# Optimization experiments

Hardware: AMD Instinct MI355X
Metric: run time of the kernel (lower is better)

## Reference

```python
import jax, jax.numpy as jnp
import numpy as np

B, T, D, H = 4, 1024, 1024, 16
DH = D // H
BETA = 0.9


def setup_inputs() -> dict:
    key = jax.random.key(0)
    ks = jax.random.split(key, 9)
    s = 1.0 / np.sqrt(D)
    return {
        "x": jax.random.normal(ks[0], (B, T, D), jnp.float32),
        "l3_memory": jax.random.normal(ks[1], (B, 1, D), jnp.float32),
        "wq": jax.random.normal(ks[2], (D, D), jnp.float32) * s,
        "wk": jax.random.normal(ks[3], (D, D), jnp.float32) * s,
        "wv": jax.random.normal(ks[4], (D, D), jnp.float32) * s,
        "wo": jax.random.normal(ks[5], (D, D), jnp.float32) * s,
        "rw1": jax.random.normal(ks[6], (D, D // 2), jnp.float32) * s,
        "rb1": jnp.zeros((D // 2,), jnp.float32),
        "rw2": jax.random.normal(ks[7], (D // 2, 3), jnp.float32) * (1.0 / np.sqrt(D // 2)),
        "rb2": jnp.zeros((3,), jnp.float32),
    }


def reference(x, l3_memory, wq, wk, wv, wo, rw1, rb1, rw2, rb2):
    b, t, d = x.shape
    dh = d // H

    def heads(y):  # [b,t,d] -> [b,h,t,dh]
        return y.reshape(b, t, H, dh).transpose(0, 2, 1, 3)

    q = x @ wq
    qh = heads(q)

    # L2: causal prefix EMA along time: y_t = beta*y_{t-1} + (1-beta)*x_t, y_{-1}=0
    def ema_step(c, xt):
        y = BETA * c + (1.0 - BETA) * xt
        return y, y
    _, l2 = jax.lax.scan(ema_step, jnp.zeros((b, d), x.dtype), jnp.swapaxes(x, 0, 1))
    l2 = jnp.swapaxes(l2, 0, 1)

    # L3: retrieval memory repeated to sequence length
    l3 = jnp.broadcast_to(l3_memory, (b, t, d))

    mask = jnp.tril(jnp.ones((t, t), bool))
    neg = jnp.finfo(x.dtype).min
    scale = 1.0 / np.sqrt(dh)

    def attend(mem):
        kh = heads(mem @ wk)
        vh = heads(mem @ wv)
        s = jnp.einsum('bhqd,bhkd->bhqk', qh, kh) * scale
        s = jnp.where(mask[None, None], s, neg)
        p = jax.nn.softmax(s, axis=-1)
        return jnp.einsum('bhqk,bhkd->bhqd', p, vh)

    # router over q tokens -> softmax mixture weights [b,t,3]
    hdn = jax.nn.gelu(q @ rw1 + rb1, approximate=False)
    lam = jax.nn.softmax(hdn @ rw2 + rb2, axis=-1)

    mixed = jnp.zeros((b, H, t, dh), x.dtype)
    for i, mem in enumerate((x, l2, l3)):
        mixed = mixed + lam[:, None, :, i:i + 1] * attend(mem)

    out = mixed.transpose(0, 2, 1, 3).reshape(b, t, d) @ wo
    return out, lam
```

## Files before the change

### kernel.cpp

```cpp
#include <hip/hip_runtime.h>
#include <hip/hip_bf16.h>
#include <math.h>


#define B_ 4
#define T_ 1024
#define D_ 1024
#define H_ 16
#define DH_ 64
#define M_ 4096

#define ECH 16
#define NCH 64

typedef __attribute__((ext_vector_type(8))) short bf16x8;
typedef __attribute__((ext_vector_type(4))) short s16x4;
typedef __attribute__((ext_vector_type(4))) float f32x4;

__device__ inline short f2b(float f) {
  __hip_bfloat16 h = __float2bfloat16(f);
  return *reinterpret_cast<short*>(&h);
}

__device__ inline void gload_lds16(const short* g, short* l) {
  __builtin_amdgcn_global_load_lds(
      (const __attribute__((address_space(1))) unsigned int*)g,
      (__attribute__((address_space(3))) unsigned int*)l, 16, 0, 0);
}

__global__ __launch_bounds__(256) void ema_chunk_kernel(const float* __restrict__ x,
                                                        float* __restrict__ l2,
                                                        short* __restrict__ xb) {
  int idx = blockIdx.x * 256 + threadIdx.x;
  int d = idx & (D_ - 1);
  int ch = (idx >> 10) & (NCH - 1);
  int b = idx >> 16;
  const float* xp = x + (size_t)(b * T_ + ch * ECH) * D_ + d;
  float* yp = l2 + (size_t)(b * T_ + ch * ECH) * D_ + d;
  short* xbp = xb + (size_t)(b * T_ + ch * ECH) * D_ + d;
  float y = 0.f;
#pragma unroll 4
  for (int t = 0; t < ECH; ++t) {
    float xv = xp[t * D_];
    y = 0.9f * y + 0.1f * xv;
    yp[t * D_] = y;
    xbp[t * D_] = f2b(xv);
  }
}

__global__ __launch_bounds__(256) void ema_carry_kernel(const float* __restrict__ l2,
                                                        float* __restrict__ g) {
  int idx = blockIdx.x * 256 + threadIdx.x;
  int d = idx & (D_ - 1);
  int b = idx >> 10;
  const float bE = 0.1853020188851841f;
  float G = 0.f;
  for (int ch = 0; ch < NCH; ++ch) {
    g[(size_t)(b * NCH + ch) * D_ + d] = G;
    float lf = l2[(size_t)(b * T_ + ch * ECH + ECH - 1) * D_ + d];
    G = lf + bE * G;
  }
}

__global__ __launch_bounds__(256) void ema_fix_kernel(const float* __restrict__ l2,
                                                      const float* __restrict__ g,
                                                      short* __restrict__ l2b) {
  int idx = blockIdx.x * 256 + threadIdx.x;
  int d = idx & (D_ - 1);
  int t = (idx >> 10) & (T_ - 1);
  int b = idx >> 20;
  int ch = t / ECH;
  int off = t & (ECH - 1);
  float G = g[(size_t)(b * NCH + ch) * D_ + d];
  float p9 = exp2f((float)(off + 1) * -0.15200309344504997f);
  l2b[idx] = f2b(l2[idx] + p9 * G);
}

__global__ __launch_bounds__(256) void transpose_w_kernel(
    const float* __restrict__ w0, const float* __restrict__ w1,
    const float* __restrict__ w2, const float* __restrict__ w3,
    const float* __restrict__ w4,
    short* __restrict__ t0, short* __restrict__ t1, short* __restrict__ t2,
    short* __restrict__ t3, short* __restrict__ t4) {
  int z = blockIdx.z;
  const float* W = (z == 0) ? w0 : (z == 1) ? w1 : (z == 2) ? w2 : (z == 3) ? w3 : w4;
  short* Wt = (z == 0) ? t0 : (z == 1) ? t1 : (z == 2) ? t2 : (z == 3) ? t3 : t4;
  int cols = (z == 4) ? 512 : 1024;
  int c0 = blockIdx.x * 32, r0 = blockIdx.y * 32;
  if (c0 >= cols) return;
  __shared__ float tile[32][33];
  int tc = threadIdx.x & 31, tr8 = threadIdx.x >> 5;
#pragma unroll
  for (int i = 0; i < 4; ++i)
    tile[tr8 + i * 8][tc] = W[(size_t)(r0 + tr8 + i * 8) * cols + c0 + tc];
  __syncthreads();
#pragma unroll
  for (int i = 0; i < 4; ++i) {
    int rr = tr8 + i * 8;
    Wt[(size_t)(c0 + rr) * 1024 + r0 + tc] = f2b(tile[tc][rr]);
  }
}

template <int NB>
__global__ __launch_bounds__(256) void gemm_bt(const short* __restrict__ A, int lda,
                                               const short* __restrict__ Bt,
                                               float* __restrict__ Cf,
                                               short* __restrict__ Cb,
                                               int Ndim, int Kdim) {
  __shared__ short As[128 * 64];
  __shared__ short Bs[NB * 64];
  constexpr int NW = NB / 64;
  constexpr int NF = 4;
  constexpr int MF = (NW == 2) ? 4 : 2;
  int tid = threadIdx.x;
  int w = tid >> 6, l = tid & 63;
  int lg = l >> 4, ll = l & 15;
  int wr = (NW == 2) ? (w >> 1) : w;
  int wc = (NW == 2) ? (w & 1) : 0;
  int row0 = blockIdx.y * 128, col0 = blockIdx.x * NB;

  f32x4 acc[MF][NF];
#pragma unroll
  for (int m = 0; m < MF; ++m)
#pragma unroll
    for (int n = 0; n < NF; ++n) acc[m][n] = (f32x4){0.f, 0.f, 0.f, 0.f};

  for (int k0 = 0; k0 < Kdim; k0 += 64) {
    __syncthreads();
#pragma unroll
    for (int it = 0; it < 4; ++it) {
      int s = it * 256 + w * 64 + l;
      int r = s >> 3;
      int c = (s & 7) ^ (r & 7);
      gload_lds16(A + (size_t)(row0 + r) * lda + k0 + c * 8, &As[(it * 256 + w * 64) * 8]);
    }
#pragma unroll
    for (int it = 0; it < NB / 32; ++it) {
      int s = it * 256 + w * 64 + l;
      int r = s >> 3;
      int c = (s & 7) ^ (r & 7);
      gload_lds16(Bt + (size_t)(col0 + r) * Kdim + k0 + c * 8, &Bs[(it * 256 + w * 64) * 8]);
    }
    __syncthreads();
#pragma unroll
    for (int ks = 0; ks < 2; ++ks) {
      bf16x8 af[MF], bfr[NF];
#pragma unroll
      for (int m = 0; m < MF; ++m) {
        int r = wr * (MF * 16) + m * 16 + ll;
        af[m] = *(const bf16x8*)&As[r * 64 + (((ks * 4 + lg) ^ (r & 7)) << 3)];
      }
#pragma unroll
      for (int n = 0; n < NF; ++n) {
        int r = wc * 64 + n * 16 + ll;
        bfr[n] = *(const bf16x8*)&Bs[r * 64 + (((ks * 4 + lg) ^ (r & 7)) << 3)];
      }
#pragma unroll
      for (int m = 0; m < MF; ++m)
#pragma unroll
        for (int n = 0; n < NF; ++n)
          acc[m][n] = __builtin_amdgcn_mfma_f32_16x16x32_bf16(af[m], bfr[n], acc[m][n], 0, 0, 0);
    }
  }
#pragma unroll
  for (int m = 0; m < MF; ++m) {
    int gr = row0 + wr * (MF * 16) + m * 16 + lg * 4;
#pragma unroll
    for (int n = 0; n < NF; ++n) {
      int gc = col0 + wc * 64 + n * 16 + ll;
#pragma unroll
      for (int r = 0; r < 4; ++r) {
        float vv = acc[m][n][r];
        if (Cf) Cf[(size_t)(gr + r) * Ndim + gc] = vv;
        if (Cb) Cb[(size_t)(gr + r) * Ndim + gc] = f2b(vv);
      }
    }
  }
}

__global__ __launch_bounds__(256) void gemm_dual(const short* __restrict__ xb,
                                                 const short* __restrict__ l2b,
                                                 const short* __restrict__ wqkvT,
                                                 short* __restrict__ QKV,
                                                 short* __restrict__ KV2) {
  int lin = blockIdx.y * 40 + blockIdx.x;
  int lin2 = (lin & 7) * 160 + (lin >> 3);
  int bx = lin2 % 40;
  int by = lin2 / 40;

  const short* A;
  const short* Bt;
  short* Cb;
  int Ndim, col0;
  if (bx < 24) {
    A = xb; Bt = wqkvT; Cb = QKV; Ndim = 3072; col0 = bx * 128;
  } else {
    A = l2b; Bt = wqkvT + 1024 * 1024; Cb = KV2; Ndim = 2048; col0 = (bx - 24) * 128;
  }
  __shared__ short As[128 * 64];
  __shared__ short Bs[128 * 64];
  int tid = threadIdx.x;
  int w = tid >> 6, l = tid & 63;
  int lg = l >> 4, ll = l & 15;
  int wr = w >> 1, wc = w & 1;
  int row0 = by * 128;

  f32x4 acc[4][4];
#pragma unroll
  for (int m = 0; m < 4; ++m)
#pragma unroll
    for (int n = 0; n < 4; ++n) acc[m][n] = (f32x4){0.f, 0.f, 0.f, 0.f};

  for (int k0 = 0; k0 < 1024; k0 += 64) {
    __syncthreads();
#pragma unroll
    for (int it = 0; it < 4; ++it) {
      int s = it * 256 + w * 64 + l;
      int r = s >> 3;
      int c = (s & 7) ^ (r & 7);
      gload_lds16(A + (size_t)(row0 + r) * 1024 + k0 + c * 8, &As[(it * 256 + w * 64) * 8]);
      gload_lds16(Bt + (size_t)(col0 + r) * 1024 + k0 + c * 8, &Bs[(it * 256 + w * 64) * 8]);
    }
    __syncthreads();
#pragma unroll
    for (int ks = 0; ks < 2; ++ks) {
      bf16x8 af[4], bfr[4];
#pragma unroll
      for (int m = 0; m < 4; ++m) {
        int r = wr * 64 + m * 16 + ll;
        af[m] = *(const bf16x8*)&As[r * 64 + (((ks * 4 + lg) ^ (r & 7)) << 3)];
      }
#pragma unroll
      for (int n = 0; n < 4; ++n) {
        int r = wc * 64 + n * 16 + ll;
        bfr[n] = *(const bf16x8*)&Bs[r * 64 + (((ks * 4 + lg) ^ (r & 7)) << 3)];
      }
#pragma unroll
      for (int m = 0; m < 4; ++m)
#pragma unroll
        for (int n = 0; n < 4; ++n)
          acc[m][n] = __builtin_amdgcn_mfma_f32_16x16x32_bf16(af[m], bfr[n], acc[m][n], 0, 0, 0);
    }
  }
#pragma unroll
  for (int m = 0; m < 4; ++m) {
    int gr = row0 + wr * 64 + m * 16 + lg * 4;
#pragma unroll
    for (int n = 0; n < 4; ++n) {
      int gc = col0 + wc * 64 + n * 16 + ll;
#pragma unroll
      for (int r = 0; r < 4; ++r)
        Cb[(size_t)(gr + r) * Ndim + gc] = f2b(acc[m][n][r]);
    }
  }
}

__global__ __launch_bounds__(256) void v3_kernel(const float* __restrict__ l3,
                                                 const float* __restrict__ wv,
                                                 float* __restrict__ v3) {
  int idx = blockIdx.x * 256 + threadIdx.x;
  int b = idx >> 10;
  int col = idx & 1023;
  const float* xr = l3 + (size_t)b * D_;
  float acc = 0.f;
#pragma unroll 8
  for (int k = 0; k < D_; ++k) acc += xr[k] * wv[(size_t)k * D_ + col];
  v3[idx] = acc;
}

__global__ __launch_bounds__(256) void router_kernel(const float* __restrict__ hdnp,
                                                     const float* __restrict__ rb1,
                                                     const float* __restrict__ rw2,
                                                     const float* __restrict__ rb2,
                                                     float* __restrict__ lam) {
  int wave = (blockIdx.x * 256 + threadIdx.x) >> 6;
  int lane = threadIdx.x & 63;
  const float* hr = hdnp + (size_t)wave * 512;
  float s0 = 0.f, s1 = 0.f, s2 = 0.f;
#pragma unroll
  for (int u = 0; u < 8; ++u) {
    int hcol = u * 64 + lane;
    float vv = hr[hcol] + rb1[hcol];
    float gl = 0.5f * vv * (1.0f + erff(vv * 0.70710678118654752f));
    s0 += gl * rw2[hcol * 3 + 0];
    s1 += gl * rw2[hcol * 3 + 1];
    s2 += gl * rw2[hcol * 3 + 2];
  }
#pragma unroll
  for (int off = 32; off; off >>= 1) {
    s0 += __shfl_xor(s0, off);
    s1 += __shfl_xor(s1, off);
    s2 += __shfl_xor(s2, off);
  }
  if (lane == 0) {
    float a = s0 + rb2[0], bb = s1 + rb2[1], c = s2 + rb2[2];
    float m = fmaxf(fmaxf(a, bb), c);
    float e0 = expf(a - m), e1 = expf(bb - m), e2 = expf(c - m);
    float inv = 1.0f / (e0 + e1 + e2);
    lam[(size_t)wave * 3 + 0] = e0 * inv;
    lam[(size_t)wave * 3 + 1] = e1 * inv;
    lam[(size_t)wave * 3 + 2] = e2 * inv;
  }
}

__global__ __launch_bounds__(256) void attn_fused_kernel(
    const short* __restrict__ q, int ldq,
    const short* __restrict__ k1, const short* __restrict__ v1, int ld1,
    const short* __restrict__ k2, const short* __restrict__ v2, int ld2,
    const float* __restrict__ lam, const float* __restrict__ v3,
    short* __restrict__ mixedb) {
  __shared__ short Ks[2][64][64];
  __shared__ short Vt[2][64][64];
  __shared__ short Ps[4][16][64];

  int bid = blockIdx.x;
  int half = bid >> 9, p = bid & 511;
  int bh = p & 63;
  int j = p >> 6;
  int qb = half ? (15 - j) : j;
  int b = bh >> 4, h = bh & 15;
  int q0 = qb * 64;
  int tid = threadIdx.x;
  int w = tid >> 6, l = tid & 63;
  int lg = l >> 4, ll = l & 15;

  int qw0 = q0 + w * 16;
  bf16x8 qf[2];
  {
    const short* qr = q + (size_t)(b * T_ + qw0 + ll) * ldq + h * DH_;
    qf[0] = *(const bf16x8*)&qr[lg * 8];
    qf[1] = *(const bf16x8*)&qr[32 + lg * 8];
  }

  float m_[2][4];
  f32x4 o[2][4];
  f32x4 ol[2];
#pragma unroll
  for (int s = 0; s < 2; ++s) {
#pragma unroll
    for (int r = 0; r < 4; ++r) m_[s][r] = -1e30f;
#pragma unroll
    for (int db = 0; db < 4; ++db) o[s][db] = (f32x4){0.f, 0.f, 0.f, 0.f};
    ol[s] = (f32x4){0.f, 0.f, 0.f, 0.f};
  }

  bf16x8 ones;
#pragma unroll
  for (int jj = 0; jj < 8; ++jj) ones[jj] = (short)0x3F80;

  const float SC = 0.125f * 1.44269504f;
  int nt = qb + 1;
  for (int t64 = 0; t64 < nt; ++t64) {
    int key0 = t64 * 64;
    __syncthreads();
#pragma unroll
    for (int s = 0; s < 2; ++s) {
      const short* kp = s ? k2 : k1;
      const short* vp = s ? v2 : v1;
      int ld = s ? ld2 : ld1;
#pragma unroll
      for (int it = 0; it < 2; ++it) {
        int e = it * 256 + w * 64 + l;
        int r = e >> 3;
        int cs = (e & 7) ^ (r & 7);
        gload_lds16(kp + (size_t)(b * T_ + key0 + r) * ld + h * DH_ + cs * 8,
                    (short*)Ks[s] + (it * 256 + w * 64) * 8);
      }
      {
        int kp2 = tid >> 3, c8 = tid & 7;
        size_t gi = (size_t)(b * T_ + key0 + kp2 * 2) * ld + h * DH_ + c8 * 8;
        bf16x8 va = *(const bf16x8*)&vp[gi];
        bf16x8 vb = *(const bf16x8*)&vp[gi + ld];
        unsigned int* Vtd = (unsigned int*)Vt[s];
#pragma unroll
        for (int jj = 0; jj < 8; ++jj) {
          int dh = c8 * 8 + jj;
          int X = ((dh ^ (dh >> 3)) & 7) << 2;
          Vtd[dh * 32 + (kp2 ^ X)] =
              ((unsigned int)(unsigned short)va[jj]) |
              (((unsigned int)(unsigned short)vb[jj]) << 16);
        }
      }
    }
    __syncthreads();
    if (key0 > qw0 + 15) continue;

#pragma unroll
    for (int s = 0; s < 2; ++s) {
      f32x4 c[4];
#pragma unroll
      for (int kt = 0; kt < 4; ++kt) c[kt] = (f32x4){0.f, 0.f, 0.f, 0.f};
      __builtin_amdgcn_s_setprio(1);
#pragma unroll
      for (int kt = 0; kt < 4; ++kt) {
        int kr = kt * 16 + ll;
        bf16x8 kfa = *(const bf16x8*)&Ks[s][kr][((lg ^ (kr & 7)) << 3)];
        bf16x8 kfb = *(const bf16x8*)&Ks[s][kr][(((4 + lg) ^ (kr & 7)) << 3)];
        c[kt] = __builtin_amdgcn_mfma_f32_16x16x32_bf16(qf[0], kfa, c[kt], 0, 0, 0);
        c[kt] = __builtin_amdgcn_mfma_f32_16x16x32_bf16(qf[1], kfb, c[kt], 0, 0, 0);
      }
      __builtin_amdgcn_s_setprio(0);

      float sv[4][4];
      if (key0 + 63 <= qw0) {
#pragma unroll
        for (int r = 0; r < 4; ++r)
#pragma unroll
          for (int kt = 0; kt < 4; ++kt) sv[r][kt] = c[kt][r] * SC;
      } else {
#pragma unroll
        for (int r = 0; r < 4; ++r) {
          int grow = qw0 + lg * 4 + r;
#pragma unroll
          for (int kt = 0; kt < 4; ++kt) {
            float t = c[kt][r] * SC;
            sv[r][kt] = (key0 + kt * 16 + ll > grow) ? -1e30f : t;
          }
        }
      }

      float mx[4];
#pragma unroll
      for (int r = 0; r < 4; ++r) {
        float m0 = fmaxf(fmaxf(sv[r][0], sv[r][1]), fmaxf(sv[r][2], sv[r][3]));
        m0 = fmaxf(m0, __shfl_xor(m0, 1));
        m0 = fmaxf(m0, __shfl_xor(m0, 2));
        m0 = fmaxf(m0, __shfl_xor(m0, 4));
        m0 = fmaxf(m0, __shfl_xor(m0, 8));
        mx[r] = m0;
      }
      int grew = 0;
#pragma unroll
      for (int r = 0; r < 4; ++r) grew |= (mx[r] > m_[s][r] + 8.f) ? 1 : 0;
      if (__any(grew)) {
#pragma unroll
        for (int r = 0; r < 4; ++r) {
          float nm = fmaxf(m_[s][r], mx[r]);
          float al = exp2f(m_[s][r] - nm);
          m_[s][r] = nm;
          ol[s][r] *= al;
#pragma unroll
          for (int db = 0; db < 4; ++db) o[s][db][r] *= al;
        }
      }

#pragma unroll
      for (int r = 0; r < 4; ++r) {
        float mr = m_[s][r];
        int prow = lg * 4 + r;
#pragma unroll
        for (int kt = 0; kt < 4; ++kt) {
          float pv = exp2f(sv[r][kt] - mr);
          Ps[w][prow][((kt ^ lg) << 4) + ll] = f2b(pv);
        }
      }
      asm volatile("s_waitcnt lgkmcnt(0)" ::: "memory");
      __builtin_amdgcn_sched_barrier(0);

      __builtin_amdgcn_s_setprio(1);
#pragma unroll
      for (int ks = 0; ks < 2; ++ks) {
        int pswz = (ks * 32 + lg * 8) ^ ((ll >> 2) << 4);
        bf16x8 pf = *(const bf16x8*)&Ps[w][ll][pswz];
        const unsigned int* Vtd = (const unsigned int*)Vt[s];
        ol[s] = __builtin_amdgcn_mfma_f32_16x16x32_bf16(pf, ones, ol[s], 0, 0, 0);
#pragma unroll
        for (int db = 0; db < 4; ++db) {
          int dh = db * 16 + ll;
          int X = ((dh ^ (dh >> 3)) & 7) << 2;
          bf16x8 vf = *(const bf16x8*)&Vtd[dh * 32 + ((ks * 16 + lg * 4) ^ X)];
          o[s][db] = __builtin_amdgcn_mfma_f32_16x16x32_bf16(pf, vf, o[s][db], 0, 0, 0);
        }
      }
      __builtin_amdgcn_s_setprio(0);
      __builtin_amdgcn_sched_barrier(0);
    }
  }

#pragma unroll
  for (int r = 0; r < 4; ++r) {
    int grow = qw0 + lg * 4 + r;
    const float* lr = lam + (size_t)(b * T_ + grow) * 3;
    float w0 = lr[0] / ol[0][r];
    float w1 = lr[1] / ol[1][r];
    float w2 = lr[2];
#pragma unroll
    for (int db = 0; db < 4; ++db) {
      int dcol = h * DH_ + db * 16 + ll;
      float val = w0 * o[0][db][r] + w1 * o[1][db][r] + w2 * v3[(b << 10) + dcol];
      mixedb[(size_t)(b * T_ + grow) * D_ + dcol] = f2b(val);
    }
  }
}

extern "C" void kernel_launch(void* const* d_in, const int* in_sizes, int n_in,
                              void* d_out, int out_size, void* d_ws, size_t ws_size,
                              hipStream_t stream) {
  const float* x = (const float*)d_in[0];
  const float* l3m = (const float*)d_in[1];
  const float* wq = (const float*)d_in[2];
  const float* wk = (const float*)d_in[3];
  const float* wv = (const float*)d_in[4];
  const float* wo = (const float*)d_in[5];
  const float* rw1 = (const float*)d_in[6];
  const float* rb1 = (const float*)d_in[7];
  const float* rw2 = (const float*)d_in[8];
  const float* rb2 = (const float*)d_in[9];

  float* out = (float*)d_out;
  float* lam = out + (size_t)M_ * D_;

  float* ws = (float*)d_ws;
  float* l2 = ws;
  short* QKV = (short*)ws;
  float* hdnp = ws + 6291456;
  float* v3 = ws + 8388608;
  float* gbuf = ws + 8392704;
  short* sb = (short*)(ws + 8654848);
  short* xb = sb;
  short* l2b = sb + 4194304;
  short* KV2 = sb + 8388608;
  short* mixedb = sb + 16777216;
  short* wqkvT = sb + 20971520;
  short* woT = sb + 24117248;
  short* rw1T = sb + 25165824;

  dim3 blk(256);

  transpose_w_kernel<<<dim3(32, 32, 5), blk, 0, stream>>>(
      wq, wk, wv, wo, rw1,
      wqkvT, wqkvT + 1024 * 1024, wqkvT + 2048 * 1024, woT, rw1T);

  ema_chunk_kernel<<<1024, blk, 0, stream>>>(x, l2, xb);
  ema_carry_kernel<<<16, blk, 0, stream>>>(l2, gbuf);
  ema_fix_kernel<<<16384, blk, 0, stream>>>(l2, gbuf, l2b);

  gemm_dual<<<dim3(40, 32), blk, 0, stream>>>(xb, l2b, wqkvT, QKV, KV2);

  gemm_bt<64><<<dim3(8, 32), blk, 0, stream>>>(QKV, 3072, rw1T, hdnp, (short*)nullptr, 512, 1024);
  router_kernel<<<1024, blk, 0, stream>>>(hdnp, rb1, rw2, rb2, lam);

  v3_kernel<<<16, blk, 0, stream>>>(l3m, wv, v3);

  attn_fused_kernel<<<1024, blk, 0, stream>>>(QKV, 3072,
                                              QKV + 1024, QKV + 2048, 3072,
                                              KV2, KV2 + 1024, 2048,
                                              lam, v3, mixedb);

  gemm_bt<64><<<dim3(16, 32), blk, 0, stream>>>(mixedb, 1024, woT, out, (short*)nullptr, 1024, 1024);
}
```

Before: 251.2 us.

## Split two-memory attention across separate blocks and sum partial outputs

The fused attention kernel now handles a single memory source (x or EMA) per block, doubling the grid to 2048 blocks. Each block keeps half the LDS and accumulator registers, which should raise occupancy and parallelism. The cost is that the two partial mixtures are written to separate bf16 buffers and combined by an extra elementwise add kernel before the output GEMM, adding memory traffic and one more bf16 rounding.

```diff
diff --git a/kernel.cpp b/kernel.cpp
--- a/kernel.cpp
+++ b/kernel.cpp
@@ -20,6 +20,11 @@
 __device__ inline short f2b(float f) {
   __hip_bfloat16 h = __float2bfloat16(f);
   return *reinterpret_cast<short*>(&h);
+}
+
+__device__ inline float b2f(unsigned short u) {
+  unsigned int x = ((unsigned int)u) << 16;
+  return *reinterpret_cast<float*>(&x);
 }
 
 __device__ inline void gload_lds16(const short* g, short* l) {
@@ -308,13 +313,15 @@
     const short* __restrict__ k1, const short* __restrict__ v1, int ld1,
     const short* __restrict__ k2, const short* __restrict__ v2, int ld2,
     const float* __restrict__ lam, const float* __restrict__ v3,
-    short* __restrict__ mixedb) {
-  __shared__ short Ks[2][64][64];
-  __shared__ short Vt[2][64][64];
+    short* __restrict__ mix0, short* __restrict__ mix1) {
+  __shared__ short Ks[64][64];
+  __shared__ short Vt[64][64];
   __shared__ short Ps[4][16][64];
 
   int bid = blockIdx.x;
-  int half = bid >> 9, p = bid & 511;
+  int s = bid >> 10;
+  int bid2 = bid & 1023;
+  int half = bid2 >> 9, p = bid2 & 511;
   int bh = p & 63;
   int j = p >> 6;
   int qb = half ? (15 - j) : j;
@@ -324,6 +331,10 @@
   int w = tid >> 6, l = tid & 63;
   int lg = l >> 4, ll = l & 15;
 
+  const short* kp = s ? k2 : k1;
+  const short* vp = s ? v2 : v1;
+  int ld = s ? ld2 : ld1;
+
   int qw0 = q0 + w * 16;
   bf16x8 qf[2];
   {
@@ -332,17 +343,14 @@
     qf[1] = *(const bf16x8*)&qr[32 + lg * 8];
   }
 
-  float m_[2][4];
-  f32x4 o[2][4];
-  f32x4 ol[2];
-#pragma unroll
-  for (int s = 0; s < 2; ++s) {
-#pragma unroll
-    for (int r = 0; r < 4; ++r) m_[s][r] = -1e30f;
-#pragma unroll
-    for (int db = 0; db < 4; ++db) o[s][db] = (f32x4){0.f, 0.f, 0.f, 0.f};
-    ol[s] = (f32x4){0.f, 0.f, 0.f, 0.f};
-  }
+  float m_[4];
+  f32x4 o[4];
+  f32x4 ol;
+#pragma unroll
+  for (int r = 0; r < 4; ++r) m_[r] = -1e30f;
+#pragma unroll
+  for (int db = 0; db < 4; ++db) o[db] = (f32x4){0.f, 0.f, 0.f, 0.f};
+  ol = (f32x4){0.f, 0.f, 0.f, 0.f};
 
   bf16x8 ones;
 #pragma unroll
@@ -354,143 +362,149 @@
     int key0 = t64 * 64;
     __syncthreads();
 #pragma unroll
-    for (int s = 0; s < 2; ++s) {
-      const short* kp = s ? k2 : k1;
-      const short* vp = s ? v2 : v1;
-      int ld = s ? ld2 : ld1;
-#pragma unroll
-      for (int it = 0; it < 2; ++it) {
-        int e = it * 256 + w * 64 + l;
-        int r = e >> 3;
-        int cs = (e & 7) ^ (r & 7);
-        gload_lds16(kp + (size_t)(b * T_ + key0 + r) * ld + h * DH_ + cs * 8,
-                    (short*)Ks[s] + (it * 256 + w * 64) * 8);
-      }
-      {
-        int kp2 = tid >> 3, c8 = tid & 7;
-        size_t gi = (size_t)(b * T_ + key0 + kp2 * 2) * ld + h * DH_ + c8 * 8;
-        bf16x8 va = *(const bf16x8*)&vp[gi];
-        bf16x8 vb = *(const bf16x8*)&vp[gi + ld];
-        unsigned int* Vtd = (unsigned int*)Vt[s];
-#pragma unroll
-        for (int jj = 0; jj < 8; ++jj) {
-          int dh = c8 * 8 + jj;
-          int X = ((dh ^ (dh >> 3)) & 7) << 2;
-          Vtd[dh * 32 + (kp2 ^ X)] =
-              ((unsigned int)(unsigned short)va[jj]) |
-              (((unsigned int)(unsigned short)vb[jj]) << 16);
-        }
+    for (int it = 0; it < 2; ++it) {
+      int e = it * 256 + w * 64 + l;
+      int r = e >> 3;
+      int cs = (e & 7) ^ (r & 7);
+      gload_lds16(kp + (size_t)(b * T_ + key0 + r) * ld + h * DH_ + cs * 8,
+                  (short*)Ks + (it * 256 + w * 64) * 8);
+    }
+    {
+      int kp2 = tid >> 3, c8 = tid & 7;
+      size_t gi = (size_t)(b * T_ + key0 + kp2 * 2) * ld + h * DH_ + c8 * 8;
+      bf16x8 va = *(const bf16x8*)&vp[gi];
+      bf16x8 vb = *(const bf16x8*)&vp[gi + ld];
+      unsigned int* Vtd = (unsigned int*)Vt;
+#pragma unroll
+      for (int jj = 0; jj < 8; ++jj) {
+        int dh = c8 * 8 + jj;
+        int X = ((dh ^ (dh >> 3)) & 7) << 2;
+        Vtd[dh * 32 + (kp2 ^ X)] =
+            ((unsigned int)(unsigned short)va[jj]) |
+            (((unsigned int)(unsigned short)vb[jj]) << 16);
       }
     }
     __syncthreads();
     if (key0 > qw0 + 15) continue;
 
-#pragma unroll
-    for (int s = 0; s < 2; ++s) {
-      f32x4 c[4];
-#pragma unroll
-      for (int kt = 0; kt < 4; ++kt) c[kt] = (f32x4){0.f, 0.f, 0.f, 0.f};
-      __builtin_amdgcn_s_setprio(1);
+    f32x4 c[4];
+#pragma unroll
+    for (int kt = 0; kt < 4; ++kt) c[kt] = (f32x4){0.f, 0.f, 0.f, 0.f};
+    __builtin_amdgcn_s_setprio(1);
+#pragma unroll
+    for (int kt = 0; kt < 4; ++kt) {
+      int kr = kt * 16 + ll;
+      bf16x8 kfa = *(const bf16x8*)&Ks[kr][((lg ^ (kr & 7)) << 3)];
+      bf16x8 kfb = *(const bf16x8*)&Ks[kr][(((4 + lg) ^ (kr & 7)) << 3)];
+      c[kt] = __builtin_amdgcn_mfma_f32_16x16x32_bf16(qf[0], kfa, c[kt], 0, 0, 0);
+      c[kt] = __builtin_amdgcn_mfma_f32_16x16x32_bf16(qf[1], kfb, c[kt], 0, 0, 0);
+    }
+    __builtin_amdgcn_s_setprio(0);
+
+    float sv[4][4];
+    if (key0 + 63 <= qw0) {
+#pragma unroll
+      for (int r = 0; r < 4; ++r)
+#pragma unroll
+        for (int kt = 0; kt < 4; ++kt) sv[r][kt] = c[kt][r] * SC;
+    } else {
+#pragma unroll
+      for (int r = 0; r < 4; ++r) {
+        int grow = qw0 + lg * 4 + r;
+#pragma unroll
+        for (int kt = 0; kt < 4; ++kt) {
+          float t = c[kt][r] * SC;
+          sv[r][kt] = (key0 + kt * 16 + ll > grow) ? -1e30f : t;
+        }
+      }
+    }
+
+    float mx[4];
+#pragma unroll
+    for (int r = 0; r < 4; ++r) {
+      float m0 = fmaxf(fmaxf(sv[r][0], sv[r][1]), fmaxf(sv[r][2], sv[r][3]));
+      m0 = fmaxf(m0, __shfl_xor(m0, 1));
+      m0 = fmaxf(m0, __shfl_xor(m0, 2));
+      m0 = fmaxf(m0, __shfl_xor(m0, 4));
+      m0 = fmaxf(m0, __shfl_xor(m0, 8));
+      mx[r] = m0;
+    }
+    int grew = 0;
+#pragma unroll
+    for (int r = 0; r < 4; ++r) grew |= (mx[r] > m_[r] + 8.f) ? 1 : 0;
+    if (__any(grew)) {
+#pragma unroll
+      for (int r = 0; r < 4; ++r) {
+        float nm = fmaxf(m_[r], mx[r]);
+        float al = exp2f(m_[r] - nm);
+        m_[r] = nm;
+        ol[r] *= al;
+#pragma unroll
+        for (int db = 0; db < 4; ++db) o[db][r] *= al;
+      }
+    }
+
+#pragma unroll
+    for (int r = 0; r < 4; ++r) {
+      float mr = m_[r];
+      int prow = lg * 4 + r;
 #pragma unroll
       for (int kt = 0; kt < 4; ++kt) {
-        int kr = kt * 16 + ll;
-        bf16x8 kfa = *(const bf16x8*)&Ks[s][kr][((lg ^ (kr & 7)) << 3)];
-        bf16x8 kfb = *(const bf16x8*)&Ks[s][kr][(((4 + lg) ^ (kr & 7)) << 3)];
-        c[kt] = __builtin_amdgcn_mfma_f32_16x16x32_bf16(qf[0], kfa, c[kt], 0, 0, 0);
-        c[kt] = __builtin_amdgcn_mfma_f32_16x16x32_bf16(qf[1], kfb, c[kt], 0, 0, 0);
-      }
-      __builtin_amdgcn_s_setprio(0);
-
-      float sv[4][4];
-      if (key0 + 63 <= qw0) {
-#pragma unroll
-        for (int r = 0; r < 4; ++r)
-#pragma unroll
-          for (int kt = 0; kt < 4; ++kt) sv[r][kt] = c[kt][r] * SC;
-      } else {
-#pragma unroll
-        for (int r = 0; r < 4; ++r) {
-          int grow = qw0 + lg * 4 + r;
-#pragma unroll
-          for (int kt = 0; kt < 4; ++kt) {
-            float t = c[kt][r] * SC;
-            sv[r][kt] = (key0 + kt * 16 + ll > grow) ? -1e30f : t;
-          }
-        }
-      }
-
-      float mx[4];
-#pragma unroll
-      for (int r = 0; r < 4; ++r) {
-        float m0 = fmaxf(fmaxf(sv[r][0], sv[r][1]), fmaxf(sv[r][2], sv[r][3]));
-        m0 = fmaxf(m0, __shfl_xor(m0, 1));
-        m0 = fmaxf(m0, __shfl_xor(m0, 2));
-        m0 = fmaxf(m0, __shfl_xor(m0, 4));
-        m0 = fmaxf(m0, __shfl_xor(m0, 8));
-        mx[r] = m0;
-      }
-      int grew = 0;
-#pragma unroll
-      for (int r = 0; r < 4; ++r) grew |= (mx[r] > m_[s][r] + 8.f) ? 1 : 0;
-      if (__any(grew)) {
-#pragma unroll
-        for (int r = 0; r < 4; ++r) {
-          float nm = fmaxf(m_[s][r], mx[r]);
-          float al = exp2f(m_[s][r] - nm);
-          m_[s][r] = nm;
-          ol[s][r] *= al;
-#pragma unroll
-          for (int db = 0; db < 4; ++db) o[s][db][r] *= al;
-        }
-      }
-
-#pragma unroll
-      for (int r = 0; r < 4; ++r) {
-        float mr = m_[s][r];
-        int prow = lg * 4 + r;
-#pragma unroll
-        for (int kt = 0; kt < 4; ++kt) {
-          float pv = exp2f(sv[r][kt] - mr);
-          Ps[w][prow][((kt ^ lg) << 4) + ll] = f2b(pv);
-        }
-      }
-      asm volatile("s_waitcnt lgkmcnt(0)" ::: "memory");
-      __builtin_amdgcn_sched_barrier(0);
-
-      __builtin_amdgcn_s_setprio(1);
-#pragma unroll
-      for (int ks = 0; ks < 2; ++ks) {
-        int pswz = (ks * 32 + lg * 8) ^ ((ll >> 2) << 4);
-        bf16x8 pf = *(const bf16x8*)&Ps[w][ll][pswz];
-        const unsigned int* Vtd = (const unsigned int*)Vt[s];
-        ol[s] = __builtin_amdgcn_mfma_f32_16x16x32_bf16(pf, ones, ol[s], 0, 0, 0);
-#pragma unroll
-        for (int db = 0; db < 4; ++db) {
-          int dh = db * 16 + ll;
-          int X = ((dh ^ (dh >> 3)) & 7) << 2;
-          bf16x8 vf = *(const bf16x8*)&Vtd[dh * 32 + ((ks * 16 + lg * 4) ^ X)];
-          o[s][db] = __builtin_amdgcn_mfma_f32_16x16x32_bf16(pf, vf, o[s][db], 0, 0, 0);
-        }
-      }
-      __builtin_amdgcn_s_setprio(0);
-      __builtin_amdgcn_sched_barrier(0);
-    }
-  }
-
+        float pv = exp2f(sv[r][kt] - mr);
+        Ps[w][prow][((kt ^ lg) << 4) + ll] = f2b(pv);
+      }
+    }
+    asm volatile("s_waitcnt lgkmcnt(0)" ::: "memory");
+    __builtin_amdgcn_sched_barrier(0);
+
+    __builtin_amdgcn_s_setprio(1);
+#pragma unroll
+    for (int ks = 0; ks < 2; ++ks) {
+      int pswz = (ks * 32 + lg * 8) ^ ((ll >> 2) << 4);
+      bf16x8 pf = *(const bf16x8*)&Ps[w][ll][pswz];
+      const unsigned int* Vtd = (const unsigned int*)Vt;
+      ol = __builtin_amdgcn_mfma_f32_16x16x32_bf16(pf, ones, ol, 0, 0, 0);
+#pragma unroll
+      for (int db = 0; db < 4; ++db) {
+        int dh = db * 16 + ll;
+        int X = ((dh ^ (dh >> 3)) & 7) << 2;
+        bf16x8 vf = *(const bf16x8*)&Vtd[dh * 32 + ((ks * 16 + lg * 4) ^ X)];
+        o[db] = __builtin_amdgcn_mfma_f32_16x16x32_bf16(pf, vf, o[db], 0, 0, 0);
+      }
+    }
+    __builtin_amdgcn_s_setprio(0);
+    __builtin_amdgcn_sched_barrier(0);
+  }
+
+  short* dst = s ? mix1 : mix0;
 #pragma unroll
   for (int r = 0; r < 4; ++r) {
     int grow = qw0 + lg * 4 + r;
     const float* lr = lam + (size_t)(b * T_ + grow) * 3;
-    float w0 = lr[0] / ol[0][r];
-    float w1 = lr[1] / ol[1][r];
+    float wgt = lr[s] / ol[r];
     float w2 = lr[2];
 #pragma unroll
     for (int db = 0; db < 4; ++db) {
       int dcol = h * DH_ + db * 16 + ll;
-      float val = w0 * o[0][db][r] + w1 * o[1][db][r] + w2 * v3[(b << 10) + dcol];
-      mixedb[(size_t)(b * T_ + grow) * D_ + dcol] = f2b(val);
-    }
-  }
+      float val = wgt * o[db][r];
+      if (s == 0) val += w2 * v3[(b << 10) + dcol];
+      dst[(size_t)(b * T_ + grow) * D_ + dcol] = f2b(val);
+    }
+  }
+}
+
+__global__ __launch_bounds__(256) void add_mix_kernel(const unsigned short* __restrict__ a,
+                                                      const unsigned short* __restrict__ b,
+                                                      short* __restrict__ c) {
+  int i = blockIdx.x * 256 + threadIdx.x;
+  ushort4 av = ((const ushort4*)a)[i];
+  ushort4 bv = ((const ushort4*)b)[i];
+  s16x4 cv;
+  cv[0] = f2b(b2f(av.x) + b2f(bv.x));
+  cv[1] = f2b(b2f(av.y) + b2f(bv.y));
+  cv[2] = f2b(b2f(av.z) + b2f(bv.z));
+  cv[3] = f2b(b2f(av.w) + b2f(bv.w));
+  ((s16x4*)c)[i] = cv;
 }
 
 extern "C" void kernel_launch(void* const* d_in, const int* in_sizes, int n_in,
@@ -520,10 +534,12 @@
   short* xb = sb;
   short* l2b = sb + 4194304;
   short* KV2 = sb + 8388608;
-  short* mixedb = sb + 16777216;
+  short* mix0 = sb + 16777216;
   short* wqkvT = sb + 20971520;
   short* woT = sb + 24117248;
   short* rw1T = sb + 25165824;
+  short* mix1 = xb;
+  short* mixs = l2b;
 
   dim3 blk(256);
 
@@ -542,10 +558,13 @@
 
   v3_kernel<<<16, blk, 0, stream>>>(l3m, wv, v3);
 
-  attn_fused_kernel<<<1024, blk, 0, stream>>>(QKV, 3072,
+  attn_fused_kernel<<<2048, blk, 0, stream>>>(QKV, 3072,
                                               QKV + 1024, QKV + 2048, 3072,
                                               KV2, KV2 + 1024, 2048,
-                                              lam, v3, mixedb);
-
-  gemm_bt<64><<<dim3(16, 32), blk, 0, stream>>>(mixedb, 1024, woT, out, (short*)nullptr, 1024, 1024);
-}
+                                              lam, v3, mix0, mix1);
+
+  add_mix_kernel<<<4096, blk, 0, stream>>>((const unsigned short*)mix0,
+                                           (const unsigned short*)mix1, mixs);
+
+  gemm_bt<64><<<dim3(16, 32), blk, 0, stream>>>(mixs, 1024, woT, out, (short*)nullptr, 1024, 1024);
+}
```

After: 256.6 us. +2.1%, slower.

## Apply EMA to K/V projections and fold router weight into QKV GEMM

Applied to the files above, without the earlier changes.

Because the EMA is linear, it commutes with the projections, so l2@Wk equals EMA(x@Wk). The change therefore runs the EMA scan over the bf16 K/V outputs instead of over x, which removes the separate l2 GEMM (N=2048, K=1024). It also precomputes Wq@rw1 as an extra 512 columns of the QKV weight, so the router hidden layer comes from the same GEMM and the standalone router GEMM goes away. In exchange, the EMA now reads bf16-rounded projections and Wq@rw1 is rounded to bf16, which changes numerical error, and the weight-product GEMM is recomputed on every call.

```diff
diff --git a/kernel.cpp b/kernel.cpp
--- a/kernel.cpp
+++ b/kernel.cpp
@@ -22,58 +22,69 @@
   return *reinterpret_cast<short*>(&h);
 }
 
+__device__ inline float b2f(unsigned short u) {
+  unsigned int x = ((unsigned int)u) << 16;
+  return *reinterpret_cast<float*>(&x);
+}
+
 __device__ inline void gload_lds16(const short* g, short* l) {
   __builtin_amdgcn_global_load_lds(
       (const __attribute__((address_space(1))) unsigned int*)g,
       (__attribute__((address_space(3))) unsigned int*)l, 16, 0, 0);
 }
 
-__global__ __launch_bounds__(256) void ema_chunk_kernel(const float* __restrict__ x,
-                                                        float* __restrict__ l2,
-                                                        short* __restrict__ xb) {
+__global__ __launch_bounds__(256) void cvt_bf16_kernel(const float* __restrict__ in,
+                                                       short* __restrict__ out) {
   int idx = blockIdx.x * 256 + threadIdx.x;
-  int d = idx & (D_ - 1);
-  int ch = (idx >> 10) & (NCH - 1);
-  int b = idx >> 16;
-  const float* xp = x + (size_t)(b * T_ + ch * ECH) * D_ + d;
-  float* yp = l2 + (size_t)(b * T_ + ch * ECH) * D_ + d;
-  short* xbp = xb + (size_t)(b * T_ + ch * ECH) * D_ + d;
+  float4 v = ((const float4*)in)[idx];
+  s16x4 o;
+  o[0] = f2b(v.x); o[1] = f2b(v.y); o[2] = f2b(v.z); o[3] = f2b(v.w);
+  ((s16x4*)out)[idx] = o;
+}
+
+__global__ __launch_bounds__(256) void ema_kv_ends_kernel(const short* __restrict__ QKV,
+                                                          float* __restrict__ ends) {
+  int idx = blockIdx.x * 256 + threadIdx.x;
+  int col = idx & 2047;
+  int ch = (idx >> 11) & (NCH - 1);
+  int b = idx >> 17;
+  const short* sp = QKV + (size_t)(b * T_ + ch * ECH) * 3584 + 1024 + col;
   float y = 0.f;
-#pragma unroll 4
-  for (int t = 0; t < ECH; ++t) {
-    float xv = xp[t * D_];
-    y = 0.9f * y + 0.1f * xv;
-    yp[t * D_] = y;
-    xbp[t * D_] = f2b(xv);
-  }
-}
-
-__global__ __launch_bounds__(256) void ema_carry_kernel(const float* __restrict__ l2,
-                                                        float* __restrict__ g) {
+#pragma unroll
+  for (int t = 0; t < ECH; ++t)
+    y = 0.9f * y + 0.1f * b2f((unsigned short)sp[(size_t)t * 3584]);
+  ends[(size_t)((b << 6) + ch) * 2048 + col] = y;
+}
+
+__global__ __launch_bounds__(256) void ema_kv_carry_kernel(float* __restrict__ ends) {
   int idx = blockIdx.x * 256 + threadIdx.x;
-  int d = idx & (D_ - 1);
-  int b = idx >> 10;
+  int col = idx & 2047;
+  int b = idx >> 11;
   const float bE = 0.1853020188851841f;
   float G = 0.f;
   for (int ch = 0; ch < NCH; ++ch) {
-    g[(size_t)(b * NCH + ch) * D_ + d] = G;
-    float lf = l2[(size_t)(b * T_ + ch * ECH + ECH - 1) * D_ + d];
-    G = lf + bE * G;
-  }
-}
-
-__global__ __launch_bounds__(256) void ema_fix_kernel(const float* __restrict__ l2,
-                                                      const float* __restrict__ g,
-                                                      short* __restrict__ l2b) {
+    size_t slot = (size_t)((b << 6) + ch) * 2048 + col;
+    float e = ends[slot];
+    ends[slot] = G;
+    G = e + bE * G;
+  }
+}
+
+__global__ __launch_bounds__(256) void ema_kv_fix_kernel(const short* __restrict__ QKV,
+                                                         const float* __restrict__ ends,
+                                                         short* __restrict__ KV2) {
   int idx = blockIdx.x * 256 + threadIdx.x;
-  int d = idx & (D_ - 1);
-  int t = (idx >> 10) & (T_ - 1);
-  int b = idx >> 20;
-  int ch = t / ECH;
-  int off = t & (ECH - 1);
-  float G = g[(size_t)(b * NCH + ch) * D_ + d];
-  float p9 = exp2f((float)(off + 1) * -0.15200309344504997f);
-  l2b[idx] = f2b(l2[idx] + p9 * G);
+  int col = idx & 2047;
+  int ch = (idx >> 11) & (NCH - 1);
+  int b = idx >> 17;
+  const short* sp = QKV + (size_t)(b * T_ + ch * ECH) * 3584 + 1024 + col;
+  short* dp = KV2 + (size_t)(b * T_ + ch * ECH) * 2048 + col;
+  float y = ends[(size_t)((b << 6) + ch) * 2048 + col];
+#pragma unroll
+  for (int t = 0; t < ECH; ++t) {
+    y = 0.9f * y + 0.1f * b2f((unsigned short)sp[(size_t)t * 3584]);
+    dp[(size_t)t * 2048] = f2b(y);
+  }
 }
 
 __global__ __launch_bounds__(256) void transpose_w_kernel(
@@ -178,83 +189,6 @@
   }
 }
 
-__global__ __launch_bounds__(256) void gemm_dual(const short* __restrict__ xb,
-                                                 const short* __restrict__ l2b,
-                                                 const short* __restrict__ wqkvT,
-                                                 short* __restrict__ QKV,
-                                                 short* __restrict__ KV2) {
-  int lin = blockIdx.y * 40 + blockIdx.x;
-  int lin2 = (lin & 7) * 160 + (lin >> 3);
-  int bx = lin2 % 40;
-  int by = lin2 / 40;
-
-  const short* A;
-  const short* Bt;
-  short* Cb;
-  int Ndim, col0;
-  if (bx < 24) {
-    A = xb; Bt = wqkvT; Cb = QKV; Ndim = 3072; col0 = bx * 128;
-  } else {
-    A = l2b; Bt = wqkvT + 1024 * 1024; Cb = KV2; Ndim = 2048; col0 = (bx - 24) * 128;
-  }
-  __shared__ short As[128 * 64];
-  __shared__ short Bs[128 * 64];
-  int tid = threadIdx.x;
-  int w = tid >> 6, l = tid & 63;
-  int lg = l >> 4, ll = l & 15;
-  int wr = w >> 1, wc = w & 1;
-  int row0 = by * 128;
-
-  f32x4 acc[4][4];
-#pragma unroll
-  for (int m = 0; m < 4; ++m)
-#pragma unroll
-    for (int n = 0; n < 4; ++n) acc[m][n] = (f32x4){0.f, 0.f, 0.f, 0.f};
-
-  for (int k0 = 0; k0 < 1024; k0 += 64) {
-    __syncthreads();
-#pragma unroll
-    for (int it = 0; it < 4; ++it) {
-      int s = it * 256 + w * 64 + l;
-      int r = s >> 3;
-      int c = (s & 7) ^ (r & 7);
-      gload_lds16(A + (size_t)(row0 + r) * 1024 + k0 + c * 8, &As[(it * 256 + w * 64) * 8]);
-      gload_lds16(Bt + (size_t)(col0 + r) * 1024 + k0 + c * 8, &Bs[(it * 256 + w * 64) * 8]);
-    }
-    __syncthreads();
-#pragma unroll
-    for (int ks = 0; ks < 2; ++ks) {
-      bf16x8 af[4], bfr[4];
-#pragma unroll
-      for (int m = 0; m < 4; ++m) {
-        int r = wr * 64 + m * 16 + ll;
-        af[m] = *(const bf16x8*)&As[r * 64 + (((ks * 4 + lg) ^ (r & 7)) << 3)];
-      }
-#pragma unroll
-      for (int n = 0; n < 4; ++n) {
-        int r = wc * 64 + n * 16 + ll;
-        bfr[n] = *(const bf16x8*)&Bs[r * 64 + (((ks * 4 + lg) ^ (r & 7)) << 3)];
-      }
-#pragma unroll
-      for (int m = 0; m < 4; ++m)
-#pragma unroll
-        for (int n = 0; n < 4; ++n)
-          acc[m][n] = __builtin_amdgcn_mfma_f32_16x16x32_bf16(af[m], bfr[n], acc[m][n], 0, 0, 0);
-    }
-  }
-#pragma unroll
-  for (int m = 0; m < 4; ++m) {
-    int gr = row0 + wr * 64 + m * 16 + lg * 4;
-#pragma unroll
-    for (int n = 0; n < 4; ++n) {
-      int gc = col0 + wc * 64 + n * 16 + ll;
-#pragma unroll
-      for (int r = 0; r < 4; ++r)
-        Cb[(size_t)(gr + r) * Ndim + gc] = f2b(acc[m][n][r]);
-    }
-  }
-}
-
 __global__ __launch_bounds__(256) void v3_kernel(const float* __restrict__ l3,
                                                  const float* __restrict__ wv,
                                                  float* __restrict__ v3) {
@@ -268,19 +202,19 @@
   v3[idx] = acc;
 }
 
-__global__ __launch_bounds__(256) void router_kernel(const float* __restrict__ hdnp,
+__global__ __launch_bounds__(256) void router_kernel(const short* __restrict__ QKV,
                                                      const float* __restrict__ rb1,
                                                      const float* __restrict__ rw2,
                                                      const float* __restrict__ rb2,
                                                      float* __restrict__ lam) {
   int wave = (blockIdx.x * 256 + threadIdx.x) >> 6;
   int lane = threadIdx.x & 63;
-  const float* hr = hdnp + (size_t)wave * 512;
+  const short* hr = QKV + (size_t)wave * 3584 + 3072;
   float s0 = 0.f, s1 = 0.f, s2 = 0.f;
 #pragma unroll
   for (int u = 0; u < 8; ++u) {
     int hcol = u * 64 + lane;
-    float vv = hr[hcol] + rb1[hcol];
+    float vv = b2f((unsigned short)hr[hcol]) + rb1[hcol];
     float gl = 0.5f * vv * (1.0f + erff(vv * 0.70710678118654752f));
     s0 += gl * rw2[hcol * 3 + 0];
     s1 += gl * rw2[hcol * 3 + 1];
@@ -511,39 +445,41 @@
   float* lam = out + (size_t)M_ * D_;
 
   float* ws = (float*)d_ws;
-  float* l2 = ws;
   short* QKV = (short*)ws;
-  float* hdnp = ws + 6291456;
-  float* v3 = ws + 8388608;
-  float* gbuf = ws + 8392704;
-  short* sb = (short*)(ws + 8654848);
+  float* v3 = ws + 7340032;
+  float* ends = ws + 7344128;
+  short* sb = (short*)(ws + 7868416);
   short* xb = sb;
-  short* l2b = sb + 4194304;
-  short* KV2 = sb + 8388608;
-  short* mixedb = sb + 16777216;
-  short* wqkvT = sb + 20971520;
-  short* woT = sb + 24117248;
-  short* rw1T = sb + 25165824;
+  short* KV2 = sb + 4194304;
+  short* mixedb = sb + 12582912;
+  short* wqkvT = sb + 16777216;
+  short* woT = sb + 20447232;
+  short* rw1T = sb + 21495808;
+  short* wqB = sb + 22020096;
 
   dim3 blk(256);
 
   transpose_w_kernel<<<dim3(32, 32, 5), blk, 0, stream>>>(
       wq, wk, wv, wo, rw1,
       wqkvT, wqkvT + 1024 * 1024, wqkvT + 2048 * 1024, woT, rw1T);
-
-  ema_chunk_kernel<<<1024, blk, 0, stream>>>(x, l2, xb);
-  ema_carry_kernel<<<16, blk, 0, stream>>>(l2, gbuf);
-  ema_fix_kernel<<<16384, blk, 0, stream>>>(l2, gbuf, l2b);
-
-  gemm_dual<<<dim3(40, 32), blk, 0, stream>>>(xb, l2b, wqkvT, QKV, KV2);
-
-  gemm_bt<64><<<dim3(8, 32), blk, 0, stream>>>(QKV, 3072, rw1T, hdnp, (short*)nullptr, 512, 1024);
-  router_kernel<<<1024, blk, 0, stream>>>(hdnp, rb1, rw2, rb2, lam);
-
+  cvt_bf16_kernel<<<4096, blk, 0, stream>>>(x, xb);
+  cvt_bf16_kernel<<<1024, blk, 0, stream>>>(wq, wqB);
+
+  gemm_bt<64><<<dim3(16, 4), blk, 0, stream>>>(rw1T, 1024, wqB, (float*)nullptr,
+                                               wqkvT + 3072 * 1024, 1024, 1024);
+
+  gemm_bt<128><<<dim3(28, 32), blk, 0, stream>>>(xb, 1024, wqkvT, (float*)nullptr,
+                                                 QKV, 3584, 1024);
+
+  ema_kv_ends_kernel<<<2048, blk, 0, stream>>>(QKV, ends);
+  ema_kv_carry_kernel<<<32, blk, 0, stream>>>(ends);
+  ema_kv_fix_kernel<<<2048, blk, 0, stream>>>(QKV, ends, KV2);
+
+  router_kernel<<<1024, blk, 0, stream>>>(QKV, rb1, rw2, rb2, lam);
   v3_kernel<<<16, blk, 0, stream>>>(l3m, wv, v3);
 
-  attn_fused_kernel<<<1024, blk, 0, stream>>>(QKV, 3072,
-                                              QKV + 1024, QKV + 2048, 3072,
+  attn_fused_kernel<<<1024, blk, 0, stream>>>(QKV, 3584,
+                                              QKV + 1024, QKV + 2048, 3584,
                                               KV2, KV2 + 1024, 2048,
                                               lam, v3, mixedb);
 
```

Measured after the change: 232.7 us. 1.08x faster.
